# Optimization experiments

Hardware: AMD Instinct MI355X
Metric: run time of the kernel (lower is better)

The kernel has to match this reference:

```python
import jax, jax.numpy as jnp
import numpy as np

N, E, D = 524288, 50000, 64
COMMITMENT_COST = 0.25
EPS = 1e-6


def setup_inputs() -> dict:
    key = jax.random.key(0)
    k1, k2, k3 = jax.random.split(key, 3)
    inputs_all = jax.random.normal(k1, (N, D + 1), dtype=jnp.float32)
    # sorted unique genus taxids (even integers) -> codebook rows 0..E-1
    genus_taxids_key = (2 * jnp.arange(E)).astype(jnp.int32)
    taxids = jax.random.randint(k2, (N,), 0, 2 * E, dtype=jnp.int32)
    lineages_all = jnp.stack([jnp.full((N,), -1, jnp.int32), taxids], axis=1)
    # original inits embeddings to zeros; use small noise so the manifold map is non-degenerate
    embeddings = 0.01 * jax.random.normal(k3, (E, D), dtype=jnp.float32)
    return {"inputs_all": inputs_all, "lineages_all": lineages_all,
            "embeddings": embeddings, "genus_taxids_key": genus_taxids_key}


def convert_codebook_lorentz(w):
    # w: [*, D] -> hyperboloid points [*, D+1]
    x = 3.0 * jnp.tanh(w)
    # Lorentz_inner_product(v, v) with v = pad(x, (1,0)) is sum(x^2)
    n = jnp.sqrt(jnp.clip(jnp.sum(x * x, axis=-1, keepdims=True), EPS, None))
    n = jnp.clip(n, None, 10.0)
    v = jnp.concatenate([jnp.zeros_like(n), x], axis=-1)          # [*, D+1]
    mu0 = jnp.concatenate([jnp.ones_like(n), jnp.zeros_like(x)], axis=-1)
    return jnp.cosh(n) * mu0 + jnp.sinh(n) * v / n


def geodesic_distance(a, b):
    lip = jnp.sum(a[..., 1:] * b[..., 1:], axis=-1) - a[..., 0] * b[..., 0]
    return jnp.arccosh(jnp.clip(-lip, 1.0 + EPS, None))


def reference(inputs_all, lineages_all, embeddings, genus_taxids_key):
    taxids = lineages_all[:, 1]
    # GPU-resident replacement of the host dict lookup: keys are sorted
    idx = jnp.searchsorted(genus_taxids_key, taxids)
    idx = jnp.clip(idx, 0, genus_taxids_key.shape[0] - 1)
    mask = genus_taxids_key[idx] == taxids                        # [N] bool, torch.isin

    quantized = convert_codebook_lorentz(embeddings[idx])         # [N, D+1]
    e_latent = geodesic_distance(jax.lax.stop_gradient(quantized), inputs_all)
    q_latent = geodesic_distance(quantized, jax.lax.stop_gradient(inputs_all))
    c_loss = q_latent + COMMITMENT_COST * e_latent                # [N]

    n_valid = jnp.maximum(jnp.sum(mask.astype(jnp.float32)), 1.0)
    mean_loss = jnp.sum(jnp.where(mask, c_loss, 0.0)) / n_valid   # mean over valid rows

    quantized_st = inputs_all + jax.lax.stop_gradient(quantized - inputs_all)
    quantized_all = jnp.where(mask[:, None], quantized_st, inputs_all)
    return mean_loss, quantized_all
```

## Files before the change

### kernel.cpp

```cpp
#include <hip/hip_runtime.h>


#define NBLOCKS 2048
#define NTHREADS 256
#define WAVES_PER_BLOCK (NTHREADS / 64)

__device__ __forceinline__ float waveReduceSum(float v) {
#pragma unroll
    for (int m = 32; m >= 1; m >>= 1) v += __shfl_xor(v, m, 64);
    return v;
}

__global__ __launch_bounds__(256) void vq_table_init(int* __restrict__ table, int ts) {
    int i = blockIdx.x * 256 + threadIdx.x;
    if (i < ts) table[i] = -1;
}

__global__ __launch_bounds__(256) void vq_table_fill(const int* __restrict__ key,
                                                     int* __restrict__ table,
                                                     int E, int ts) {
    int i = blockIdx.x * 256 + threadIdx.x;
    if (i < E) {
        int k = key[i];
        if ((unsigned)k < (unsigned)ts) table[k] = i;
    }
}

__device__ __forceinline__ float fast_tanh(float x) {
    x = fminf(fmaxf(x, -15.0f), 15.0f);
    float e2 = __expf(2.0f * x);
    return (e2 - 1.0f) * __builtin_amdgcn_rcpf(e2 + 1.0f);
}

__global__ __launch_bounds__(NTHREADS) void vq_main(
    const float* __restrict__ inputs,
    const int*   __restrict__ lineages,
    const float* __restrict__ emb,
    const int*   __restrict__ table,
    float* __restrict__ out,
    float* __restrict__ partialLoss,
    float* __restrict__ partialCnt,
    int N, int ts)
{
    const int lane        = threadIdx.x & 63;
    const int waveInBlock = threadIdx.x >> 6;
    const int waveGlobal  = blockIdx.x * WAVES_PER_BLOCK + waveInBlock;
    const int totalWaves  = gridDim.x * WAVES_PER_BLOCK;

    float lossAcc = 0.0f;
    float cntAcc  = 0.0f;

    for (int row = waveGlobal; row < N; row += totalWaves) {
        const int t = lineages[2 * (size_t)row + 1];
        const int idx = ((unsigned)t < (unsigned)ts) ? table[t] : -1;
        const bool match = (idx >= 0);

        const float* inRow = inputs + (size_t)row * 65;
        const float in0 = inRow[0];
        const float ind = inRow[1 + lane];
        float* outRow = out + 1 + (size_t)row * 65;

        if (match) {
            const float w = emb[(size_t)idx * 64 + lane];
            const float x = 3.0f * fast_tanh(w);
            float n2 = waveReduceSum(x * x);
            n2 = fmaxf(n2, 1e-6f);
            float n = sqrtf(n2);
            n = fminf(n, 10.0f);
            const float e  = __expf(n);
            const float ei = __builtin_amdgcn_rcpf(e);
            const float c  = 0.5f * (e + ei);
            const float s  = 0.5f * (e - ei) * __builtin_amdgcn_rcpf(n);
            const float qd = s * x;
            const float dot = waveReduceSum(qd * ind);
            const float lip = dot - c * in0;
            const float z = fmaxf(-lip, 1.0f + 1e-6f);
            const float dist = __logf(z + sqrtf(fmaxf(z * z - 1.0f, 0.0f)));
            if (lane == 0) { lossAcc += 1.25f * dist; cntAcc += 1.0f; }
            outRow[1 + lane] = qd;
            if (lane == 0) outRow[0] = c;
        } else {
            outRow[1 + lane] = ind;
            if (lane == 0) outRow[0] = in0;
        }
    }

    __shared__ float sLoss[WAVES_PER_BLOCK];
    __shared__ float sCnt[WAVES_PER_BLOCK];
    if (lane == 0) { sLoss[waveInBlock] = lossAcc; sCnt[waveInBlock] = cntAcc; }
    __syncthreads();
    if (threadIdx.x == 0) {
        float L = 0.0f, C = 0.0f;
#pragma unroll
        for (int i = 0; i < WAVES_PER_BLOCK; i++) { L += sLoss[i]; C += sCnt[i]; }
        partialLoss[blockIdx.x] = L;
        partialCnt[blockIdx.x]  = C;
    }
}

__global__ __launch_bounds__(256) void vq_finalize(
    const float* __restrict__ partialLoss,
    const float* __restrict__ partialCnt,
    float* __restrict__ out, int nParts)
{
    __shared__ float sL[256];
    __shared__ float sC[256];
    float L = 0.0f, C = 0.0f;
    for (int i = threadIdx.x; i < nParts; i += 256) {
        L += partialLoss[i];
        C += partialCnt[i];
    }
    sL[threadIdx.x] = L; sC[threadIdx.x] = C;
    __syncthreads();
    if (threadIdx.x == 0) {
        float tl = 0.0f, tc = 0.0f;
        for (int i = 0; i < 256; i++) { tl += sL[i]; tc += sC[i]; }
        out[0] = tl / fmaxf(tc, 1.0f);
    }
}

extern "C" void kernel_launch(void* const* d_in, const int* in_sizes, int n_in,
                              void* d_out, int out_size, void* d_ws, size_t ws_size,
                              hipStream_t stream) {
    const float* inputs   = (const float*)d_in[0];
    const int*   lineages = (const int*)d_in[1];
    const float* emb      = (const float*)d_in[2];
    const int*   key      = (const int*)d_in[3];
    const int E = in_sizes[3];
    const int N = in_sizes[0] / 65;
    const int ts = 2 * E;

    float* out = (float*)d_out;
    int*   table = (int*)d_ws;
    float* partialLoss = (float*)((char*)d_ws + (size_t)ts * sizeof(int));
    float* partialCnt  = partialLoss + NBLOCKS;

    vq_table_init<<<(ts + 255) / 256, 256, 0, stream>>>(table, ts);
    vq_table_fill<<<(E + 255) / 256, 256, 0, stream>>>(key, table, E, ts);
    vq_main<<<NBLOCKS, NTHREADS, 0, stream>>>(inputs, lineages, emb, table,
                                              out, partialLoss, partialCnt, N, ts);
    vq_finalize<<<1, 256, 0, stream>>>(partialLoss, partialCnt, out, NBLOCKS);
}
```

Before: 344.9 us.

## Precompute Lorentz codebook once and process two rows per wave iteration

A new kernel converts every embedding row to its hyperboloid point once and writes a 65-float codebook to workspace. The main kernel then gathers precomputed rows instead of redoing the tanh, norm reduction and cosh/sinh for each matching input row. The main loop also handles two rows per iteration (row and row+half) so more independent loads are in flight at once. The cost is an extra kernel launch, an extra pass over the codebook, more workspace, and an assumption that N is even (the loop bound is N>>1).

```diff
diff --git a/kernel.cpp b/kernel.cpp
--- a/kernel.cpp
+++ b/kernel.cpp
@@ -9,6 +9,12 @@
 #pragma unroll
     for (int m = 32; m >= 1; m >>= 1) v += __shfl_xor(v, m, 64);
     return v;
+}
+
+__device__ __forceinline__ float fast_tanh(float x) {
+    x = fminf(fmaxf(x, -15.0f), 15.0f);
+    float e2 = __expf(2.0f * x);
+    return (e2 - 1.0f) * __builtin_amdgcn_rcpf(e2 + 1.0f);
 }
 
 __global__ __launch_bounds__(256) void vq_table_init(int* __restrict__ table, int ts) {
@@ -26,16 +32,65 @@
     }
 }
 
-__device__ __forceinline__ float fast_tanh(float x) {
-    x = fminf(fmaxf(x, -15.0f), 15.0f);
-    float e2 = __expf(2.0f * x);
-    return (e2 - 1.0f) * __builtin_amdgcn_rcpf(e2 + 1.0f);
+__global__ __launch_bounds__(256) void vq_codebook(const float* __restrict__ emb,
+                                                   float* __restrict__ cb, int E) {
+    const int lane = threadIdx.x & 63;
+    const int wave = (blockIdx.x * NTHREADS + threadIdx.x) >> 6;
+    if (wave >= E) return;
+    const float w = emb[(size_t)wave * 64 + lane];
+    const float x = 3.0f * fast_tanh(w);
+    float n2 = waveReduceSum(x * x);
+    n2 = fmaxf(n2, 1e-6f);
+    float n = fminf(sqrtf(n2), 10.0f);
+    const float e  = __expf(n);
+    const float ei = __builtin_amdgcn_rcpf(e);
+    const float c  = 0.5f * (e + ei);
+    const float s  = 0.5f * (e - ei) * __builtin_amdgcn_rcpf(n);
+    float* cbRow = cb + (size_t)wave * 65;
+    cbRow[1 + lane] = s * x;
+    if (lane == 0) cbRow[0] = c;
+}
+
+struct RowCtx {
+    const float* inputs;
+    const int*   lineages;
+    const float* cb;
+    const int*   table;
+    float*       out;
+    int          ts;
+};
+
+__device__ __forceinline__ void process_row(const RowCtx& c, int row, int lane,
+                                            float& lossAcc, float& cntAcc) {
+    const int t = c.lineages[2 * (size_t)row + 1];
+    const int idx = ((unsigned)t < (unsigned)c.ts) ? c.table[t] : -1;
+
+    const float* inRow = c.inputs + (size_t)row * 65;
+    const float in0 = inRow[0];
+    const float ind = inRow[1 + lane];
+    float* outRow = c.out + 1 + (size_t)row * 65;
+
+    if (idx >= 0) {
+        const float* cbRow = c.cb + (size_t)idx * 65;
+        const float cc = cbRow[0];
+        const float qd = cbRow[1 + lane];
+        const float dot = waveReduceSum(qd * ind);
+        const float lip = dot - cc * in0;
+        const float z = fmaxf(-lip, 1.0f + 1e-6f);
+        const float dist = __logf(z + sqrtf(fmaxf(z * z - 1.0f, 0.0f)));
+        if (lane == 0) { lossAcc += 1.25f * dist; cntAcc += 1.0f; }
+        outRow[1 + lane] = qd;
+        if (lane == 0) outRow[0] = cc;
+    } else {
+        outRow[1 + lane] = ind;
+        if (lane == 0) outRow[0] = in0;
+    }
 }
 
 __global__ __launch_bounds__(NTHREADS) void vq_main(
     const float* __restrict__ inputs,
     const int*   __restrict__ lineages,
-    const float* __restrict__ emb,
+    const float* __restrict__ cb,
     const int*   __restrict__ table,
     float* __restrict__ out,
     float* __restrict__ partialLoss,
@@ -46,43 +101,14 @@
     const int waveInBlock = threadIdx.x >> 6;
     const int waveGlobal  = blockIdx.x * WAVES_PER_BLOCK + waveInBlock;
     const int totalWaves  = gridDim.x * WAVES_PER_BLOCK;
+    const int half        = N >> 1;
 
-    float lossAcc = 0.0f;
-    float cntAcc  = 0.0f;
+    RowCtx c{inputs, lineages, cb, table, out, ts};
+    float lossAcc = 0.0f, cntAcc = 0.0f;
 
-    for (int row = waveGlobal; row < N; row += totalWaves) {
-        const int t = lineages[2 * (size_t)row + 1];
-        const int idx = ((unsigned)t < (unsigned)ts) ? table[t] : -1;
-        const bool match = (idx >= 0);
-
-        const float* inRow = inputs + (size_t)row * 65;
-        const float in0 = inRow[0];
-        const float ind = inRow[1 + lane];
-        float* outRow = out + 1 + (size_t)row * 65;
-
-        if (match) {
-            const float w = emb[(size_t)idx * 64 + lane];
-            const float x = 3.0f * fast_tanh(w);
-            float n2 = waveReduceSum(x * x);
-            n2 = fmaxf(n2, 1e-6f);
-            float n = sqrtf(n2);
-            n = fminf(n, 10.0f);
-            const float e  = __expf(n);
-            const float ei = __builtin_amdgcn_rcpf(e);
-            const float c  = 0.5f * (e + ei);
-            const float s  = 0.5f * (e - ei) * __builtin_amdgcn_rcpf(n);
-            const float qd = s * x;
-            const float dot = waveReduceSum(qd * ind);
-            const float lip = dot - c * in0;
-            const float z = fmaxf(-lip, 1.0f + 1e-6f);
-            const float dist = __logf(z + sqrtf(fmaxf(z * z - 1.0f, 0.0f)));
-            if (lane == 0) { lossAcc += 1.25f * dist; cntAcc += 1.0f; }
-            outRow[1 + lane] = qd;
-            if (lane == 0) outRow[0] = c;
-        } else {
-            outRow[1 + lane] = ind;
-            if (lane == 0) outRow[0] = in0;
-        }
+    for (int row = waveGlobal; row < half; row += totalWaves) {
+        process_row(c, row,        lane, lossAcc, cntAcc);
+        process_row(c, row + half, lane, lossAcc, cntAcc);
     }
 
     __shared__ float sLoss[WAVES_PER_BLOCK];
@@ -131,13 +157,16 @@
     const int ts = 2 * E;
 
     float* out = (float*)d_out;
-    int*   table = (int*)d_ws;
-    float* partialLoss = (float*)((char*)d_ws + (size_t)ts * sizeof(int));
+    char*  ws  = (char*)d_ws;
+    int*   table = (int*)ws;
+    float* cb    = (float*)(ws + (size_t)ts * sizeof(int));
+    float* partialLoss = cb + (size_t)E * 65;
     float* partialCnt  = partialLoss + NBLOCKS;
 
     vq_table_init<<<(ts + 255) / 256, 256, 0, stream>>>(table, ts);
     vq_table_fill<<<(E + 255) / 256, 256, 0, stream>>>(key, table, E, ts);
-    vq_main<<<NBLOCKS, NTHREADS, 0, stream>>>(inputs, lineages, emb, table,
+    vq_codebook<<<(E * 64 + NTHREADS - 1) / NTHREADS, NTHREADS, 0, stream>>>(emb, cb, E);
+    vq_main<<<NBLOCKS, NTHREADS, 0, stream>>>(inputs, lineages, cb, table,
                                               out, partialLoss, partialCnt, N, ts);
     vq_finalize<<<1, 256, 0, stream>>>(partialLoss, partialCnt, out, NBLOCKS);
 }
```

After: 375.3 us. 1.09x slower.
